# Kernel optimization log

Measured on AMD Instinct MI355X. Metric: run time of the kernel, lower is better.

The kernel has to match this reference:

```python
import jax, jax.numpy as jnp
import numpy as np

TRI_PLANE_AXES = np.array([
    [[1, 0, 0], [0, 1, 0], [0, 0, 1]],
    [[1, 0, 0], [0, 0, 1], [0, 1, 0]],
    [[0, 0, 1], [0, 1, 0], [1, 0, 0]],
], dtype=np.float32)


def _grid_sample_bilinear(img, ix, iy):
    # img: [C,H,W]; ix, iy: [M] unnormalized pixel coords.
    # Matches torch grid_sample(mode='bilinear', padding_mode='zeros', align_corners=False).
    C, H, W = img.shape
    x0f = jnp.floor(ix)
    y0f = jnp.floor(iy)
    wx = ix - x0f
    wy = iy - y0f
    x0 = x0f.astype(jnp.int32)
    y0 = y0f.astype(jnp.int32)

    def gather(yi, xi):
        valid = (xi >= 0) & (xi < W) & (yi >= 0) & (yi < H)
        v = img[:, jnp.clip(yi, 0, H - 1), jnp.clip(xi, 0, W - 1)]  # [C,M]
        return v * valid.astype(img.dtype)

    v00 = gather(y0, x0)
    v01 = gather(y0, x0 + 1)
    v10 = gather(y0 + 1, x0)
    v11 = gather(y0 + 1, x0 + 1)
    return (v00 * (1 - wy) * (1 - wx) + v01 * (1 - wy) * wx
            + v10 * wy * (1 - wx) + v11 * wy * wx)  # [C,M]


def setup_inputs() -> dict:
    key = jax.random.key(0)
    k1, k2 = jax.random.split(key)
    N, M = 4, 131072
    C, S = 64, 512
    coords = jax.random.uniform(k1, (N, M, 3), jnp.float32, minval=-1.0, maxval=1.0)
    tplanes = jax.random.uniform(k2, (1, 3, C, S, S), jnp.float32, minval=-0.01, maxval=0.01)
    return {"coords": coords, "tplanes": tplanes}


def reference(coords, tplanes):
    N, M, _ = coords.shape
    _, n_planes, C, H, W = tplanes.shape
    inv_planes = jnp.linalg.inv(jnp.asarray(TRI_PLANE_AXES))  # [3,3,3] (tiny)
    # projections[..., :2]: coords @ inv_plane per plane
    proj = jnp.einsum('nmc,pcd->npmd', coords, inv_planes)[..., :2]  # [N,3,M,2]
    gx, gy = proj[..., 0], proj[..., 1]
    # align_corners=False unnormalization
    ix = ((gx + 1.0) * W - 1.0) * 0.5
    iy = ((gy + 1.0) * H - 1.0) * 0.5
    imgs = jnp.broadcast_to(tplanes, (N, n_planes, C, H, W)).reshape(N * n_planes, C, H, W)
    feats = jax.vmap(_grid_sample_bilinear)(
        imgs, ix.reshape(N * n_planes, M), iy.reshape(N * n_planes, M))  # [N*3,C,M]
    feats = feats.reshape(N, n_planes, C, M).transpose(0, 3, 1, 2)  # [N,M,3,C]
    return feats.reshape(N, M, n_planes * C)  # concat over planes
```

## Files before the change

kernel.cpp:

```cpp
#include <hip/hip_runtime.h>
#include <hip/hip_fp16.h>

namespace {

constexpr int S = 512;
constexpr int C = 64;
constexpr int TILE = 16;
constexpr int TPP  = 32;
constexpr int NBINS = 3 * TPP * TPP;
constexpr int CAP = 744;
constexpr int OVF_CAP = 8192;
constexpr int BIN_IT = 4;

constexpr int HH = 17;
constexpr int HW = 17;
constexpr int TSTRIDE = 72;
constexpr int LDSH = HH * HW * TSTRIDE;

typedef float f32x4 __attribute__((ext_vector_type(4)));
struct alignas(8) H4 { __half2 a, b; };
typedef unsigned long long u64;

__device__ __forceinline__ unsigned quantg(float g)
{
    float v = (g + 1.0f) * 262144.0f;
    int q = (int)floorf(v);
    q = min(max(q, 0), 1048575);
    return (unsigned)q;
}

__device__ __forceinline__ int x0_of_q(unsigned q) { return ((int)q - 512) >> 10; }

__device__ __forceinline__ int bin_from_q(int p, unsigned qx, unsigned qy)
{
    int xc0 = min(max(x0_of_q(qx), 0), S - 1);
    int yc0 = min(max(x0_of_q(qy), 0), S - 1);
    return p * (TPP * TPP) + (yc0 >> 4) * TPP + (xc0 >> 4);
}

__global__ __launch_bounds__(512) void tp_bin(const float* __restrict__ coords,
                                              int total_s,
                                              int* __restrict__ bincnt,
                                              u64* __restrict__ slots,
                                              u64* __restrict__ ovf,
                                              int* __restrict__ ovf_cnt)
{
    __shared__ int lh[NBINS];
    __shared__ int lbase[NBINS];
    int t = threadIdx.x;
    for (int i = t; i < NBINS; i += 512) lh[i] = 0;
    __syncthreads();
    int base = blockIdx.x * (512 * BIN_IT);

    for (int it = 0; it < BIN_IT; ++it) {
        int s = base + it * 512 + t;
        if (s < total_s) {
            float cx = coords[3 * s], cy = coords[3 * s + 1], cz = coords[3 * s + 2];
            #pragma unroll
            for (int p = 0; p < 3; ++p) {
                float gx = (p == 2) ? cz : cx;
                float gy = (p == 1) ? cz : cy;
                atomicAdd(&lh[bin_from_q(p, quantg(gx), quantg(gy))], 1);
            }
        }
    }
    __syncthreads();
    for (int i = t; i < NBINS; i += 512) {
        int c = lh[i];
        if (c) lbase[i] = atomicAdd(&bincnt[i], c);
    }
    __syncthreads();
    for (int i = t; i < NBINS; i += 512) lh[i] = 0;
    __syncthreads();

    for (int it = 0; it < BIN_IT; ++it) {
        int s = base + it * 512 + t;
        if (s < total_s) {
            float cx = coords[3 * s], cy = coords[3 * s + 1], cz = coords[3 * s + 2];
            #pragma unroll
            for (int p = 0; p < 3; ++p) {
                float gx = (p == 2) ? cz : cx;
                float gy = (p == 1) ? cz : cy;
                unsigned qx = quantg(gx), qy = quantg(gy);
                int bn = bin_from_q(p, qx, qy);
                int r  = atomicAdd(&lh[bn], 1);
                int slot = lbase[bn] + r;
                u64 rec = ((u64)(3 * s + p) << 40) | ((u64)qy << 20) | qx;
                if (slot < CAP) {
                    slots[(size_t)bn * CAP + slot] = rec;
                } else {
                    int o = atomicAdd(ovf_cnt, 1);
                    if (o < OVF_CAP) ovf[o] = rec;
                }
            }
        }
    }
}

__global__ __launch_bounds__(512) void tp_sample_tiled(const float* __restrict__ tp,
                                                       const int* __restrict__ bincnt,
                                                       const u64* __restrict__ slots,
                                                       float* __restrict__ out)
{
    __shared__ __half tile[LDSH] __attribute__((aligned(16)));

    int b0i = blockIdx.x;
    int b = (b0i & 7) * (NBINS / 8) + (b0i >> 3);

    int p  = b >> 10;
    int ty = (b >> 5) & 31;
    int tx = b & 31;
    int xg = tx * TILE;
    int yg = ty * TILE;

    const float* pl = tp + (size_t)p * C * (S * S);

    for (int task = threadIdx.x; task < C * HH * 5; task += 512) {
        int seg = task % 5;
        int rem = task / 5;
        int row = rem % HH;
        int ch  = rem / HH;
        int y   = min(yg + row, S - 1);
        int cb  = (seg < 4) ? seg * 4 : 13;
        int xb  = xg + cb;
        if (xb > S - 4) xb = S - 4;
        float4 v = *reinterpret_cast<const float4*>(pl + ((size_t)ch * S + y) * S + xb);
        __half* trow = &tile[(row * HW) * TSTRIDE + ch];
        #pragma unroll
        for (int i = 0; i < 4; ++i) {
            int col = xb + i - xg;
            if (col >= 0 && col < HW)
                trow[col * TSTRIDE] = __float2half(((const float*)&v)[i]);
        }
        if (xb != xg + cb)
            trow[16 * TSTRIDE] = __float2half(((const float*)&v)[3]);
    }
    __syncthreads();

    int cnt = min(bincnt[b], CAP);
    const u64* sb = slots + (size_t)b * CAP;
    int grp = threadIdx.x >> 3;
    int t   = threadIdx.x & 7;

    for (int gi = grp; gi < cnt; gi += 64) {
        u64 rec = sb[gi];
        int sp = (int)(rec >> 40);
        unsigned qx = (unsigned)rec & 0xFFFFFu;
        unsigned qy = (unsigned)(rec >> 20) & 0xFFFFFu;

        float ix = (float)qx * (1.0f / 1024.0f) - 0.5f;
        float iy = (float)qy * (1.0f / 1024.0f) - 0.5f;
        int x0 = x0_of_q(qx), y0 = x0_of_q(qy);
        float wx = ix - (float)x0, wy = iy - (float)y0;
        int x1 = x0 + 1, y1 = y0 + 1;

        bool vx0 = ((unsigned)x0 < (unsigned)S);
        bool vx1 = ((unsigned)x1 < (unsigned)S);
        bool vy0 = ((unsigned)y0 < (unsigned)S);
        bool vy1 = ((unsigned)y1 < (unsigned)S);

        float w00 = (vx0 && vy0) ? (1.0f - wy) * (1.0f - wx) : 0.0f;
        float w01 = (vx1 && vy0) ? (1.0f - wy) * wx          : 0.0f;
        float w10 = (vx0 && vy1) ? wy * (1.0f - wx)          : 0.0f;
        float w11 = (vx1 && vy1) ? wy * wx                   : 0.0f;

        int lx0 = min(max(x0, 0), S - 1) - xg;
        int lx1 = min(max(x1, 0), S - 1) - xg;
        int ly0 = min(max(y0, 0), S - 1) - yg;
        int ly1 = min(max(y1, 0), S - 1) - yg;

        int o00 = (ly0 * HW + lx0) * TSTRIDE;
        int o01 = (ly0 * HW + lx1) * TSTRIDE;
        int o10 = (ly1 * HW + lx0) * TSTRIDE;
        int o11 = (ly1 * HW + lx1) * TSTRIDE;

        #pragma unroll
        for (int h = 0; h < 2; ++h) {
            int c = 4 * t + 32 * h;
            H4 v00 = *reinterpret_cast<const H4*>(&tile[o00 + c]);
            H4 v01 = *reinterpret_cast<const H4*>(&tile[o01 + c]);
            H4 v10 = *reinterpret_cast<const H4*>(&tile[o10 + c]);
            H4 v11 = *reinterpret_cast<const H4*>(&tile[o11 + c]);

            float2 a  = __half22float2(v00.a), a2 = __half22float2(v00.b);
            float2 bb = __half22float2(v01.a), b2 = __half22float2(v01.b);
            float2 cc = __half22float2(v10.a), c2 = __half22float2(v10.b);
            float2 d  = __half22float2(v11.a), d2 = __half22float2(v11.b);

            f32x4 r;
            r.x = w00 * a.x  + w01 * bb.x + w10 * cc.x + w11 * d.x;
            r.y = w00 * a.y  + w01 * bb.y + w10 * cc.y + w11 * d.y;
            r.z = w00 * a2.x + w01 * b2.x + w10 * c2.x + w11 * d2.x;
            r.w = w00 * a2.y + w01 * b2.y + w10 * c2.y + w11 * d2.y;

            __builtin_nontemporal_store(r, reinterpret_cast<f32x4*>(out + (size_t)sp * 64 + c));
        }
    }
}

__global__ __launch_bounds__(256) void tp_overflow(const float* __restrict__ tp,
                                                   const u64* __restrict__ ovf,
                                                   const int* __restrict__ ovf_cnt,
                                                   float* __restrict__ out)
{
    int tid = blockIdx.x * 256 + threadIdx.x;
    int e = tid >> 4;
    int cnt = min(*ovf_cnt, OVF_CAP);
    if (e >= cnt) return;
    int t = tid & 15;

    u64 rec = ovf[e];
    int sp = (int)(rec >> 40);
    unsigned qx = (unsigned)rec & 0xFFFFFu;
    unsigned qy = (unsigned)(rec >> 20) & 0xFFFFFu;
    int p = sp - 3 * (sp / 3);

    float ix = (float)qx * (1.0f / 1024.0f) - 0.5f;
    float iy = (float)qy * (1.0f / 1024.0f) - 0.5f;
    int x0 = x0_of_q(qx), y0 = x0_of_q(qy);
    float wx = ix - (float)x0, wy = iy - (float)y0;
    int x1 = x0 + 1, y1 = y0 + 1;

    bool vx0 = ((unsigned)x0 < (unsigned)S);
    bool vx1 = ((unsigned)x1 < (unsigned)S);
    bool vy0 = ((unsigned)y0 < (unsigned)S);
    bool vy1 = ((unsigned)y1 < (unsigned)S);

    float w00 = (vx0 && vy0) ? (1.0f - wy) * (1.0f - wx) : 0.0f;
    float w01 = (vx1 && vy0) ? (1.0f - wy) * wx          : 0.0f;
    float w10 = (vx0 && vy1) ? wy * (1.0f - wx)          : 0.0f;
    float w11 = (vx1 && vy1) ? wy * wx                   : 0.0f;

    int xc0 = min(max(x0, 0), S - 1), xc1 = min(max(x1, 0), S - 1);
    int yc0 = min(max(y0, 0), S - 1), yc1 = min(max(y1, 0), S - 1);

    int o00 = yc0 * S + xc0, o01 = yc0 * S + xc1;
    int o10 = yc1 * S + xc0, o11 = yc1 * S + xc1;

    const float* pb = tp + (size_t)p * C * (S * S);
    float r[4];
    #pragma unroll
    for (int j = 0; j < 4; ++j) {
        const float* ch = pb + (size_t)(4 * t + j) * (S * S);
        r[j] = w00 * ch[o00] + w01 * ch[o01] + w10 * ch[o10] + w11 * ch[o11];
    }
    float4 v = make_float4(r[0], r[1], r[2], r[3]);
    *reinterpret_cast<float4*>(out + (size_t)sp * 64 + 4 * t) = v;
}

__global__ __launch_bounds__(256) void tp_sample_direct(const float* __restrict__ coords,
                                                        const float* __restrict__ tp,
                                                        float* __restrict__ out,
                                                        int total_sp)
{
    int tid = blockIdx.x * 256 + threadIdx.x;
    int gi = tid >> 4;
    if (gi >= total_sp) return;
    int t = tid & 15;

    int s = gi / 3;
    int p = gi - 3 * s;
    float cx = coords[3 * s], cy = coords[3 * s + 1], cz = coords[3 * s + 2];
    float gx = (p == 2) ? cz : cx;
    float gy = (p == 1) ? cz : cy;
    float ix = (gx + 1.0f) * 256.0f - 0.5f;
    float iy = (gy + 1.0f) * 256.0f - 0.5f;

    float x0f = floorf(ix), y0f = floorf(iy);
    float wx = ix - x0f, wy = iy - y0f;
    int x0 = (int)x0f, y0 = (int)y0f;
    int x1 = x0 + 1,   y1 = y0 + 1;

    bool vx0 = ((unsigned)x0 < (unsigned)S);
    bool vx1 = ((unsigned)x1 < (unsigned)S);
    bool vy0 = ((unsigned)y0 < (unsigned)S);
    bool vy1 = ((unsigned)y1 < (unsigned)S);

    float w00 = (vx0 && vy0) ? (1.0f - wy) * (1.0f - wx) : 0.0f;
    float w01 = (vx1 && vy0) ? (1.0f - wy) * wx          : 0.0f;
    float w10 = (vx0 && vy1) ? wy * (1.0f - wx)          : 0.0f;
    float w11 = (vx1 && vy1) ? wy * wx                   : 0.0f;

    int xc0 = min(max(x0, 0), S - 1), xc1 = min(max(x1, 0), S - 1);
    int yc0 = min(max(y0, 0), S - 1), yc1 = min(max(y1, 0), S - 1);

    int o00 = yc0 * S + xc0, o01 = yc0 * S + xc1;
    int o10 = yc1 * S + xc0, o11 = yc1 * S + xc1;

    const float* pb = tp + (size_t)p * C * (S * S);
    float r[4];
    #pragma unroll
    for (int j = 0; j < 4; ++j) {
        const float* ch = pb + (size_t)(4 * t + j) * (S * S);
        r[j] = w00 * ch[o00] + w01 * ch[o01] + w10 * ch[o10] + w11 * ch[o11];
    }
    float4 v = make_float4(r[0], r[1], r[2], r[3]);
    *reinterpret_cast<float4*>(out + (size_t)gi * 64 + 4 * t) = v;
}

}

extern "C" void kernel_launch(void* const* d_in, const int* in_sizes, int n_in,
                              void* d_out, int out_size, void* d_ws, size_t ws_size,
                              hipStream_t stream)
{
    const float* coords  = (const float*)d_in[0];
    const float* tplanes = (const float*)d_in[1];
    float* out = (float*)d_out;

    int total_sp = in_sizes[0];
    int total_s  = total_sp / 3;

    const size_t bincntOff = 0;
    const size_t ovfcntOff = (size_t)NBINS * 4;
    const size_t ovfOff    = 12352;
    const size_t slotsOff  = ovfOff + (size_t)OVF_CAP * 8;
    const size_t need      = slotsOff + (size_t)NBINS * CAP * 8;

    if (ws_size >= need) {
        int* bincnt  = (int*)((char*)d_ws + bincntOff);
        int* ovf_cnt = (int*)((char*)d_ws + ovfcntOff);
        u64* ovf     = (u64*)((char*)d_ws + ovfOff);
        u64* slots   = (u64*)((char*)d_ws + slotsOff);

        int nb_bin = (total_s + 512 * BIN_IT - 1) / (512 * BIN_IT);
        int nb_ovf = (OVF_CAP * 16) / 256;

        hipMemsetAsync(d_ws, 0, ovfcntOff + 64, stream);
        tp_bin<<<nb_bin, 512, 0, stream>>>(coords, total_s, bincnt, slots, ovf, ovf_cnt);
        tp_sample_tiled<<<NBINS, 512, 0, stream>>>(tplanes, bincnt, slots, out);
        tp_overflow<<<nb_ovf, 256, 0, stream>>>(tplanes, ovf, ovf_cnt, out);
    } else {
        int nb_sm = (total_sp * 16 + 255) / 256;
        tp_sample_direct<<<nb_sm, 256, 0, stream>>>(coords, tplanes, out, total_sp);
    }
}
```

Measured before the change: 135.0 us.

## Cache bin records in registers, fold overflow into sampler, shrink LDS stride

The binning kernel now keeps each sample's bin index and packed record in registers from the counting pass, so the scatter pass no longer reloads coordinates or recomputes quantisation. The separate overflow kernel is removed and its work is done by block 0 of the tiled sampler, which saves one launch. The LDS tile stride drops from 72 to 68 halves, reducing shared memory per block but possibly changing bank-conflict behaviour. Folding overflow into one block could serialise that work if overflow is large, and it relies on the overflow buffer already being complete when block 0 reads it.

```diff
diff --git a/kernel.cpp b/kernel.cpp
--- a/kernel.cpp
+++ b/kernel.cpp
@@ -14,7 +14,7 @@
 
 constexpr int HH = 17;
 constexpr int HW = 17;
-constexpr int TSTRIDE = 72;
+constexpr int TSTRIDE = 68;
 constexpr int LDSH = HH * HW * TSTRIDE;
 
 typedef float f32x4 __attribute__((ext_vector_type(4)));
@@ -52,29 +52,14 @@
     __syncthreads();
     int base = blockIdx.x * (512 * BIN_IT);
 
+    int  bn [BIN_IT][3];
+    u64  rec[BIN_IT][3];
+
+    #pragma unroll
     for (int it = 0; it < BIN_IT; ++it) {
         int s = base + it * 512 + t;
-        if (s < total_s) {
-            float cx = coords[3 * s], cy = coords[3 * s + 1], cz = coords[3 * s + 2];
-            #pragma unroll
-            for (int p = 0; p < 3; ++p) {
-                float gx = (p == 2) ? cz : cx;
-                float gy = (p == 1) ? cz : cy;
-                atomicAdd(&lh[bin_from_q(p, quantg(gx), quantg(gy))], 1);
-            }
-        }
-    }
-    __syncthreads();
-    for (int i = t; i < NBINS; i += 512) {
-        int c = lh[i];
-        if (c) lbase[i] = atomicAdd(&bincnt[i], c);
-    }
-    __syncthreads();
-    for (int i = t; i < NBINS; i += 512) lh[i] = 0;
-    __syncthreads();
-
-    for (int it = 0; it < BIN_IT; ++it) {
-        int s = base + it * 512 + t;
+        #pragma unroll
+        for (int p = 0; p < 3; ++p) bn[it][p] = -1;
         if (s < total_s) {
             float cx = coords[3 * s], cy = coords[3 * s + 1], cz = coords[3 * s + 2];
             #pragma unroll
@@ -82,15 +67,35 @@
                 float gx = (p == 2) ? cz : cx;
                 float gy = (p == 1) ? cz : cy;
                 unsigned qx = quantg(gx), qy = quantg(gy);
-                int bn = bin_from_q(p, qx, qy);
-                int r  = atomicAdd(&lh[bn], 1);
-                int slot = lbase[bn] + r;
-                u64 rec = ((u64)(3 * s + p) << 40) | ((u64)qy << 20) | qx;
+                int b = bin_from_q(p, qx, qy);
+                bn[it][p]  = b;
+                rec[it][p] = ((u64)(3 * s + p) << 40) | ((u64)qy << 20) | qx;
+                atomicAdd(&lh[b], 1);
+            }
+        }
+    }
+    __syncthreads();
+    for (int i = t; i < NBINS; i += 512) {
+        int c = lh[i];
+        if (c) lbase[i] = atomicAdd(&bincnt[i], c);
+    }
+    __syncthreads();
+    for (int i = t; i < NBINS; i += 512) lh[i] = 0;
+    __syncthreads();
+
+    #pragma unroll
+    for (int it = 0; it < BIN_IT; ++it) {
+        #pragma unroll
+        for (int p = 0; p < 3; ++p) {
+            int b = bn[it][p];
+            if (b >= 0) {
+                int r = atomicAdd(&lh[b], 1);
+                int slot = lbase[b] + r;
                 if (slot < CAP) {
-                    slots[(size_t)bn * CAP + slot] = rec;
+                    slots[(size_t)b * CAP + slot] = rec[it][p];
                 } else {
                     int o = atomicAdd(ovf_cnt, 1);
-                    if (o < OVF_CAP) ovf[o] = rec;
+                    if (o < OVF_CAP) ovf[o] = rec[it][p];
                 }
             }
         }
@@ -100,6 +105,8 @@
 __global__ __launch_bounds__(512) void tp_sample_tiled(const float* __restrict__ tp,
                                                        const int* __restrict__ bincnt,
                                                        const u64* __restrict__ slots,
+                                                       const u64* __restrict__ ovf,
+                                                       const int* __restrict__ ovf_cnt,
                                                        float* __restrict__ out)
 {
     __shared__ __half tile[LDSH] __attribute__((aligned(16)));
@@ -196,56 +203,52 @@
             __builtin_nontemporal_store(r, reinterpret_cast<f32x4*>(out + (size_t)sp * 64 + c));
         }
     }
-}
-
-__global__ __launch_bounds__(256) void tp_overflow(const float* __restrict__ tp,
-                                                   const u64* __restrict__ ovf,
-                                                   const int* __restrict__ ovf_cnt,
-                                                   float* __restrict__ out)
-{
-    int tid = blockIdx.x * 256 + threadIdx.x;
-    int e = tid >> 4;
-    int cnt = min(*ovf_cnt, OVF_CAP);
-    if (e >= cnt) return;
-    int t = tid & 15;
-
-    u64 rec = ovf[e];
-    int sp = (int)(rec >> 40);
-    unsigned qx = (unsigned)rec & 0xFFFFFu;
-    unsigned qy = (unsigned)(rec >> 20) & 0xFFFFFu;
-    int p = sp - 3 * (sp / 3);
-
-    float ix = (float)qx * (1.0f / 1024.0f) - 0.5f;
-    float iy = (float)qy * (1.0f / 1024.0f) - 0.5f;
-    int x0 = x0_of_q(qx), y0 = x0_of_q(qy);
-    float wx = ix - (float)x0, wy = iy - (float)y0;
-    int x1 = x0 + 1, y1 = y0 + 1;
-
-    bool vx0 = ((unsigned)x0 < (unsigned)S);
-    bool vx1 = ((unsigned)x1 < (unsigned)S);
-    bool vy0 = ((unsigned)y0 < (unsigned)S);
-    bool vy1 = ((unsigned)y1 < (unsigned)S);
-
-    float w00 = (vx0 && vy0) ? (1.0f - wy) * (1.0f - wx) : 0.0f;
-    float w01 = (vx1 && vy0) ? (1.0f - wy) * wx          : 0.0f;
-    float w10 = (vx0 && vy1) ? wy * (1.0f - wx)          : 0.0f;
-    float w11 = (vx1 && vy1) ? wy * wx                   : 0.0f;
-
-    int xc0 = min(max(x0, 0), S - 1), xc1 = min(max(x1, 0), S - 1);
-    int yc0 = min(max(y0, 0), S - 1), yc1 = min(max(y1, 0), S - 1);
-
-    int o00 = yc0 * S + xc0, o01 = yc0 * S + xc1;
-    int o10 = yc1 * S + xc0, o11 = yc1 * S + xc1;
-
-    const float* pb = tp + (size_t)p * C * (S * S);
-    float r[4];
-    #pragma unroll
-    for (int j = 0; j < 4; ++j) {
-        const float* ch = pb + (size_t)(4 * t + j) * (S * S);
-        r[j] = w00 * ch[o00] + w01 * ch[o01] + w10 * ch[o10] + w11 * ch[o11];
-    }
-    float4 v = make_float4(r[0], r[1], r[2], r[3]);
-    *reinterpret_cast<float4*>(out + (size_t)sp * 64 + 4 * t) = v;
+
+    if (b0i == 0) {
+        int ocnt = min(*ovf_cnt, OVF_CAP);
+        for (int e = grp; e < ocnt; e += 64) {
+            u64 rec = ovf[e];
+            int sp = (int)(rec >> 40);
+            unsigned qx = (unsigned)rec & 0xFFFFFu;
+            unsigned qy = (unsigned)(rec >> 20) & 0xFFFFFu;
+            int pp = sp - 3 * (sp / 3);
+
+            float ix = (float)qx * (1.0f / 1024.0f) - 0.5f;
+            float iy = (float)qy * (1.0f / 1024.0f) - 0.5f;
+            int x0 = x0_of_q(qx), y0 = x0_of_q(qy);
+            float wx = ix - (float)x0, wy = iy - (float)y0;
+            int x1 = x0 + 1, y1 = y0 + 1;
+
+            bool vx0 = ((unsigned)x0 < (unsigned)S);
+            bool vx1 = ((unsigned)x1 < (unsigned)S);
+            bool vy0 = ((unsigned)y0 < (unsigned)S);
+            bool vy1 = ((unsigned)y1 < (unsigned)S);
+
+            float w00 = (vx0 && vy0) ? (1.0f - wy) * (1.0f - wx) : 0.0f;
+            float w01 = (vx1 && vy0) ? (1.0f - wy) * wx          : 0.0f;
+            float w10 = (vx0 && vy1) ? wy * (1.0f - wx)          : 0.0f;
+            float w11 = (vx1 && vy1) ? wy * wx                   : 0.0f;
+
+            int xc0 = min(max(x0, 0), S - 1), xc1 = min(max(x1, 0), S - 1);
+            int yc0 = min(max(y0, 0), S - 1), yc1 = min(max(y1, 0), S - 1);
+
+            int o00 = yc0 * S + xc0, o01 = yc0 * S + xc1;
+            int o10 = yc1 * S + xc0, o11 = yc1 * S + xc1;
+
+            const float* pb = tp + (size_t)pp * C * (S * S);
+            #pragma unroll
+            for (int h = 0; h < 2; ++h) {
+                float r[4];
+                #pragma unroll
+                for (int j = 0; j < 4; ++j) {
+                    const float* ch = pb + (size_t)(4 * t + 32 * h + j) * (S * S);
+                    r[j] = w00 * ch[o00] + w01 * ch[o01] + w10 * ch[o10] + w11 * ch[o11];
+                }
+                float4 v = make_float4(r[0], r[1], r[2], r[3]);
+                *reinterpret_cast<float4*>(out + (size_t)sp * 64 + 4 * t + 32 * h) = v;
+            }
+        }
+    }
 }
 
 __global__ __launch_bounds__(256) void tp_sample_direct(const float* __restrict__ coords,
@@ -324,12 +327,10 @@
         u64* slots   = (u64*)((char*)d_ws + slotsOff);
 
         int nb_bin = (total_s + 512 * BIN_IT - 1) / (512 * BIN_IT);
-        int nb_ovf = (OVF_CAP * 16) / 256;
 
         hipMemsetAsync(d_ws, 0, ovfcntOff + 64, stream);
         tp_bin<<<nb_bin, 512, 0, stream>>>(coords, total_s, bincnt, slots, ovf, ovf_cnt);
-        tp_sample_tiled<<<NBINS, 512, 0, stream>>>(tplanes, bincnt, slots, out);
-        tp_overflow<<<nb_ovf, 256, 0, stream>>>(tplanes, ovf, ovf_cnt, out);
+        tp_sample_tiled<<<NBINS, 512, 0, stream>>>(tplanes, bincnt, slots, ovf, ovf_cnt, out);
     } else {
         int nb_sm = (total_sp * 16 + 255) / 256;
         tp_sample_direct<<<nb_sm, 256, 0, stream>>>(coords, tplanes, out, total_sp);
```

After: 133.0 us. Within noise of the previous version (-1.5%).
